# Kernel optimization log

Hardware: AMD Instinct MI355X
Metric: run time of the kernel (lower is better)

## Reference

```python
import jax, jax.numpy as jnp
import numpy as np

B, L, T = 256, 256, 50  # batch, max_len, num_tags


def setup_inputs() -> dict:
    key = jax.random.key(0)
    k1, k2, k3 = jax.random.split(key, 3)
    feats = jax.random.normal(k1, (B, L, T), dtype=jnp.float32)
    trans_m = jax.random.normal(k2, (T, T), dtype=jnp.float32)
    tags = jax.random.randint(k3, (B, L), 0, T)
    mask = jnp.ones((B, L), dtype=jnp.int32)
    return {"feats": feats, "trans_m": trans_m, "tags": tags, "mask": mask}


def _normalizer(logits, trans_m, m):
    # logits: (L, B, T), m: (L, B) float mask
    alpha0 = logits[0]  # (B, T)

    def step(alpha, inp):
        emit, mt = inp  # (B, T), (B,)
        # (B, T_from, T_to) broadcast add, logsumexp over T_from
        tmp = alpha[:, :, None] + trans_m[None, :, :] + emit[:, None, :]
        new = jax.nn.logsumexp(tmp, axis=1)
        alpha = jnp.where(mt[:, None] > 0, new, alpha)
        return alpha, None

    alpha, _ = jax.lax.scan(step, alpha0, (logits[1:], m[1:]))
    return jax.nn.logsumexp(alpha, axis=1)  # (B,)


def _gold_score(logits, trans_m, tags_t, m):
    # logits: (L, B, T); tags_t: (L, B); m: (L, B)
    trans_sc = trans_m[tags_t[:-1], tags_t[1:]] * m[1:]  # (L-1, B)
    emit_sc = jnp.take_along_axis(logits, tags_t[:, :, None], axis=2)[..., 0] * m  # (L, B)
    return jnp.sum(trans_sc + emit_sc[:-1], axis=0) + emit_sc[-1]  # (B,)


def reference(feats, trans_m, tags, mask):
    # feats: (B, L, T) -> (L, B, T); include_start_end_trans=False
    logits = jnp.transpose(feats, (1, 0, 2))
    tags_t = tags.T
    m = mask.T.astype(feats.dtype)
    all_path = _normalizer(logits, trans_m, m)
    gold = _gold_score(logits, trans_m, tags_t, m)
    return all_path - gold  # (B,) loss per example
```

## Files before the change

### kernel.cpp

```cpp
#include <hip/hip_runtime.h>
#include <math.h>


#define TAGS 50
#define LEN 256
#define NB 256
#define TOTF (NB * LEN * TAGS)
#define INV_LN2 1.4426950408889634f
#define LN2 0.6931471805599453f

typedef __attribute__((ext_vector_type(8))) short bf16x8;
typedef __attribute__((ext_vector_type(4))) float f32x4;
typedef __attribute__((ext_vector_type(4), aligned(4))) float f32x4u;

#if __has_builtin(__builtin_amdgcn_exp2f)
#define EXP2F(x) __builtin_amdgcn_exp2f(x)
#else
#define EXP2F(x) exp2f(x)
#endif
#if __has_builtin(__builtin_amdgcn_logf)
#define LOG2F(x) __builtin_amdgcn_logf(x)
#else
#define LOG2F(x) log2f(x)
#endif
#if __has_builtin(__builtin_amdgcn_rcpf)
#define RCPF(x) __builtin_amdgcn_rcpf(x)
#else
#define RCPF(x) (1.0f / (x))
#endif

__device__ __forceinline__ float readlane_f(float v, int srclane) {
  return __builtin_bit_cast(float,
      __builtin_amdgcn_readlane(__builtin_bit_cast(int, v), srclane));
}

__device__ __forceinline__ int bf16pairInit(float lo, float hi) {
  unsigned lb = (__builtin_bit_cast(unsigned, lo) + 0x8000u) >> 16;
  unsigned hb = (__builtin_bit_cast(unsigned, hi) + 0x8000u) & 0xFFFF0000u;
  return (int)(hb | lb);
}

__device__ __forceinline__ float bf16f(unsigned short u) {
  return __builtin_bit_cast(float, ((unsigned)u) << 16);
}

#define PACK2(dst, lo, hi) \
  asm("v_cvt_pk_bf16_f32 %0, %1, %2" : "=v"(dst) : "v"(lo), "v"(hi))

union U8 { int i[4]; bf16x8 v; };

__global__ __launch_bounds__(512, 1) void crf_seg_kernel(
    const float* __restrict__ feats,
    const float* __restrict__ trans,
    const int*   __restrict__ tags,
    const int*   __restrict__ mask,
    float*       __restrict__ out)
{
  const int b    = blockIdx.x;
  const int tid  = threadIdx.x;
  const int w    = tid >> 6;
  const int lane = tid & 63;
  const int q    = lane >> 4;
  const int n    = lane & 15;

  __shared__ __align__(16) unsigned short Plds[6][64][64];
  __shared__ __align__(16) float u_lds[64];
  __shared__ __align__(16) float w_lds[64];
  __shared__ float Sseg[8];
  __shared__ float norm_s, gold_s;

  const int* mbp = mask + b * LEN;
  const unsigned long long mb0 = __ballot(mbp[lane] > 0);
  const unsigned long long mb1 = __ballot(mbp[64 + lane] > 0);
  const unsigned long long mb2 = __ballot(mbp[128 + lane] > 0);
  const unsigned long long mb3 = __ballot(mbp[192 + lane] > 0);
#define MASKBIT(L)                                                          \
  ((int)(((((L) & 128) ? (((L) & 64) ? mb3 : mb2)                           \
                       : (((L) & 64) ? mb1 : mb0)) >> ((L) & 63)) & 1ull))

  U8 Afr[4][2];
#pragma unroll
  for (int t = 0; t < 4; ++t)
#pragma unroll
    for (int c = 0; c < 2; ++c)
#pragma unroll
      for (int r = 0; r < 4; ++r) {
        const int col = 16 * t + n;
        const int tag0 = 16 * c + 4 * q + r;
        const int tag1 = tag0 + 32;
        float e0 = 0.0f, e1 = 0.0f;
        if (col < TAGS) {
          if (tag0 < TAGS) e0 = EXP2F(trans[tag0 * TAGS + col] * INV_LN2);
          if (tag1 < TAGS) e1 = EXP2F(trans[tag1 * TAGS + col] * INV_LN2);
        }
        Afr[t][c].i[r] = bf16pairInit(e0, e1);
      }

  const f32x4 zero4 = {0.0f, 0.0f, 0.0f, 0.0f};

  f32x4 d[4][4];
#pragma unroll
  for (int J = 0; J < 4; ++J)
#pragma unroll
    for (int I = 0; I < 4; ++I)
#pragma unroll
      for (int r = 0; r < 4; ++r)
        d[J][I][r] = (16 * J + n == 16 * I + 4 * q + r) ? 1.0f : 0.0f;

  const int l0 = 32 * w + 1;
  float S = 0.0f;
  f32x4u rA[4], rB[4];

#define LOADG(BK, L) do {                                                   \
    const float* _p = feats + (size_t)b * (LEN * TAGS) + (size_t)(L) * TAGS;\
    BK[0] = *(const f32x4u*)(_p + 4 * q);                                   \
    BK[1] = *(const f32x4u*)(_p + 16 + 4 * q);                              \
    BK[2] = *(const f32x4u*)(_p + 32 + 4 * q);                              \
    const float* _p3 = _p + 46 + 4 * q;                                     \
    const float* _lim = feats + (TOTF - 4);                                 \
    if (_p3 > _lim) _p3 = _lim;                                             \
    BK[3] = *(const f32x4u*)_p3;                                            \
  } while (0)

#define RENORMM() do {                                                      \
    const float _cc = readlane_f(d[0][0][0], 0);                            \
    const float _rr = RCPF(_cc);                                            \
    S += LOG2F(_cc);                                                        \
    _Pragma("unroll") for (int _J = 0; _J < 4; ++_J)                        \
    _Pragma("unroll") for (int _I = 0; _I < 4; ++_I)                        \
    _Pragma("unroll") for (int _r = 0; _r < 4; ++_r)                        \
      d[_J][_I][_r] *= _rr;                                                 \
  } while (0)

#define STEPM(EH, L) do {                                                   \
    if (MASKBIT(L)) {                                                       \
      float ev[4][4];                                                       \
      _Pragma("unroll") for (int _i = 0; _i < 3; ++_i)                      \
      _Pragma("unroll") for (int _r = 0; _r < 4; ++_r)                      \
        ev[_i][_r] = EXP2F(EH[_i][_r] * INV_LN2);                           \
      ev[3][0] = EXP2F(EH[3][2] * INV_LN2);                                 \
      ev[3][1] = EXP2F(EH[3][3] * INV_LN2);                                 \
      ev[3][2] = 0.0f; ev[3][3] = 0.0f;                                     \
      _Pragma("unroll") for (int _J = 0; _J < 4; ++_J) {                    \
        U8 B0, B1;                                                          \
        _Pragma("unroll") for (int _r = 0; _r < 4; ++_r) {                  \
          PACK2(B0.i[_r], d[_J][0][_r], d[_J][2][_r]);                      \
          PACK2(B1.i[_r], d[_J][1][_r], d[_J][3][_r]);                      \
        }                                                                   \
        f32x4 t0 = __builtin_amdgcn_mfma_f32_16x16x32_bf16(Afr[0][1].v, B1.v, zero4, 0, 0, 0); \
        f32x4 t1 = __builtin_amdgcn_mfma_f32_16x16x32_bf16(Afr[1][1].v, B1.v, zero4, 0, 0, 0); \
        f32x4 t2 = __builtin_amdgcn_mfma_f32_16x16x32_bf16(Afr[2][1].v, B1.v, zero4, 0, 0, 0); \
        f32x4 t3 = __builtin_amdgcn_mfma_f32_16x16x32_bf16(Afr[3][1].v, B1.v, zero4, 0, 0, 0); \
        t0 = __builtin_amdgcn_mfma_f32_16x16x32_bf16(Afr[0][0].v, B0.v, t0, 0, 0, 0); \
        t1 = __builtin_amdgcn_mfma_f32_16x16x32_bf16(Afr[1][0].v, B0.v, t1, 0, 0, 0); \
        t2 = __builtin_amdgcn_mfma_f32_16x16x32_bf16(Afr[2][0].v, B0.v, t2, 0, 0, 0); \
        t3 = __builtin_amdgcn_mfma_f32_16x16x32_bf16(Afr[3][0].v, B0.v, t3, 0, 0, 0); \
        _Pragma("unroll") for (int _r = 0; _r < 4; ++_r) {                  \
          d[_J][0][_r] = t0[_r] * ev[0][_r];                                \
          d[_J][1][_r] = t1[_r] * ev[1][_r];                                \
          d[_J][2][_r] = t2[_r] * ev[2][_r];                                \
          d[_J][3][_r] = t3[_r] * ev[3][_r];                                \
        }                                                                   \
      }                                                                     \
    }                                                                       \
  } while (0)

  LOADG(rA, l0);
  LOADG(rB, l0 + 1);

  for (int k = 0; k < 15; ++k) {
    const int l = l0 + 2 * k;
    if ((k & 1) == 0) RENORMM();
    STEPM(rA, l);
    { const int rl = (l + 2 < 255) ? l + 2 : 255; LOADG(rA, rl); }
    STEPM(rB, l + 1);
    { const int rl = (l + 3 < 255) ? l + 3 : 255; LOADG(rB, rl); }
  }
  STEPM(rA, l0 + 30);
  if (w != 7) STEPM(rB, l0 + 31);

  if (lane == 0) Sseg[w] = S;

  if (w == 0) {
    float v0v[4];
#pragma unroll
    for (int J = 0; J < 4; ++J) {
      const int tg = 16 * J + n;
      const float f = feats[(size_t)b * (LEN * TAGS) + tg];
      v0v[J] = (tg < TAGS) ? EXP2F(f * INV_LN2) : 0.0f;
    }
    float pu[4][4];
#pragma unroll
    for (int I = 0; I < 4; ++I)
#pragma unroll
      for (int r = 0; r < 4; ++r)
        pu[I][r] = v0v[0] * d[0][I][r] + v0v[1] * d[1][I][r] +
                   v0v[2] * d[2][I][r] + v0v[3] * d[3][I][r];
#pragma unroll
    for (int off = 1; off <= 8; off <<= 1)
#pragma unroll
      for (int I = 0; I < 4; ++I)
#pragma unroll
        for (int r = 0; r < 4; ++r)
          pu[I][r] += __shfl_xor(pu[I][r], off, 64);
    if (n == 0) {
#pragma unroll
      for (int I = 0; I < 4; ++I)
#pragma unroll
        for (int r = 0; r < 4; ++r)
          u_lds[16 * I + 4 * q + r] = pu[I][r];
    }
  } else if (w == 7) {
    float pw[4];
#pragma unroll
    for (int J = 0; J < 4; ++J) {
      float s = 0.0f;
#pragma unroll
      for (int I = 0; I < 4; ++I)
#pragma unroll
        for (int r = 0; r < 4; ++r)
          s += d[J][I][r];
      pw[J] = s;
    }
#pragma unroll
    for (int J = 0; J < 4; ++J) {
      pw[J] += __shfl_xor(pw[J], 16, 64);
      pw[J] += __shfl_xor(pw[J], 32, 64);
    }
    if (q == 0) {
#pragma unroll
      for (int J = 0; J < 4; ++J) w_lds[16 * J + n] = pw[J];
    }
  } else {
#pragma unroll
    for (int J = 0; J < 4; ++J)
#pragma unroll
      for (int I = 0; I < 4; ++I) {
        int lo, hi;
        PACK2(lo, d[J][I][0], d[J][I][1]);
        PACK2(hi, d[J][I][2], d[J][I][3]);
        unsigned* dst = (unsigned*)&Plds[w - 1][16 * J + n][16 * I + 4 * q];
        dst[0] = (unsigned)lo;
        dst[1] = (unsigned)hi;
      }
  }

  __syncthreads();

  if (w == 0) {
    float x = u_lds[lane];
    float stot = 0.0f;
    for (int j = 0; j < 6; ++j) {
      u_lds[lane] = x;
      asm volatile("s_waitcnt lgkmcnt(0)" ::: "memory");
      float y0 = 0.0f, y1 = 0.0f, y2 = 0.0f, y3 = 0.0f;
#pragma unroll 4
      for (int r = 0; r < 64; r += 4) {
        y0 += u_lds[r]     * bf16f(Plds[j][r][lane]);
        y1 += u_lds[r + 1] * bf16f(Plds[j][r + 1][lane]);
        y2 += u_lds[r + 2] * bf16f(Plds[j][r + 2][lane]);
        y3 += u_lds[r + 3] * bf16f(Plds[j][r + 3][lane]);
      }
      float y = (y0 + y1) + (y2 + y3);
      const float cc = readlane_f(y, 0);
      stot += LOG2F(cc);
      x = y * RCPF(cc);
      asm volatile("s_waitcnt lgkmcnt(0)" ::: "memory");
    }
    float dotv = x * w_lds[lane];
#pragma unroll
    for (int off = 32; off; off >>= 1) dotv += __shfl_xor(dotv, off, 64);
    if (lane == 0) {
      float Ssum = 0.0f;
#pragma unroll
      for (int i = 0; i < 8; ++i) Ssum += Sseg[i];
      norm_s = LN2 * (Ssum + stot + LOG2F(dotv));
    }
  } else if (w == 1) {
    const float* fb = feats + (size_t)b * (LEN * TAGS);
    const int* tb = tags + b * LEN;
    float gp = 0.0f;
#pragma unroll
    for (int k = 0; k < 4; ++k) {
      const int p = lane + 64 * k;
      const int tg = tb[p];
      if (mbp[p] > 0) {
        float vv = fb[p * TAGS + tg];
        if (p >= 1) vv += trans[tb[p - 1] * TAGS + tg];
        gp += vv;
      }
    }
#pragma unroll
    for (int off = 32; off; off >>= 1) gp += __shfl_xor(gp, off, 64);
    if (lane == 0) gold_s = gp;
  }

  __syncthreads();
  if (tid == 0) out[b] = norm_s - gold_s;

#undef MASKBIT
#undef LOADG
#undef RENORMM
#undef STEPM
}

extern "C" void kernel_launch(void* const* d_in, const int* in_sizes, int n_in,
                              void* d_out, int out_size, void* d_ws, size_t ws_size,
                              hipStream_t stream) {
  const float* feats = (const float*)d_in[0];
  const float* trans = (const float*)d_in[1];
  const int*   tags  = (const int*)d_in[2];
  const int*   mask  = (const int*)d_in[3];
  float* out = (float*)d_out;
  (void)d_ws; (void)ws_size;

  crf_seg_kernel<<<NB, 512, 0, stream>>>(feats, trans, tags, mask, out);
}
```

Measured before the change: 106.1 us.

## Split CRF normalizer into forward and backward half-chains with separate combine kernel

```diff
diff --git a/kernel.cpp b/kernel.cpp
--- a/kernel.cpp
+++ b/kernel.cpp
@@ -40,34 +40,33 @@
   return (int)(hb | lb);
 }
 
-__device__ __forceinline__ float bf16f(unsigned short u) {
-  return __builtin_bit_cast(float, ((unsigned)u) << 16);
-}
-
 #define PACK2(dst, lo, hi) \
   asm("v_cvt_pk_bf16_f32 %0, %1, %2" : "=v"(dst) : "v"(lo), "v"(hi))
 
 union U8 { int i[4]; bf16x8 v; };
 
-__global__ __launch_bounds__(512, 1) void crf_seg_kernel(
+#define WS_U(b)  ((b) * 64)
+#define WS_W(b)  ((NB + (b)) * 64)
+#define WS_SF(b) (2 * NB * 64 + (b))
+#define WS_SB(b) (2 * NB * 64 + NB + (b))
+
+__global__ __launch_bounds__(512, 4) void crf_seg_kernel(
     const float* __restrict__ feats,
     const float* __restrict__ trans,
-    const int*   __restrict__ tags,
     const int*   __restrict__ mask,
-    float*       __restrict__ out)
+    float*       __restrict__ ws)
 {
-  const int b    = blockIdx.x;
-  const int tid  = threadIdx.x;
-  const int w    = tid >> 6;
-  const int lane = tid & 63;
-  const int q    = lane >> 4;
-  const int n    = lane & 15;
-
-  __shared__ __align__(16) unsigned short Plds[6][64][64];
-  __shared__ __align__(16) float u_lds[64];
-  __shared__ __align__(16) float w_lds[64];
+  const int bid    = blockIdx.x;
+  const bool is_fwd = bid < NB;
+  const int b      = is_fwd ? bid : bid - NB;
+  const int tid    = threadIdx.x;
+  const int w      = tid >> 6;
+  const int lane   = tid & 63;
+  const int q      = lane >> 4;
+  const int n      = lane & 15;
+
+  __shared__ __align__(16) float x_lds[64];
   __shared__ float Sseg[8];
-  __shared__ float norm_s, gold_s;
 
   const int* mbp = mask + b * LEN;
   const unsigned long long mb0 = __ballot(mbp[lane] > 0);
@@ -90,8 +89,12 @@
         const int tag1 = tag0 + 32;
         float e0 = 0.0f, e1 = 0.0f;
         if (col < TAGS) {
-          if (tag0 < TAGS) e0 = EXP2F(trans[tag0 * TAGS + col] * INV_LN2);
-          if (tag1 < TAGS) e1 = EXP2F(trans[tag1 * TAGS + col] * INV_LN2);
+          if (tag0 < TAGS)
+            e0 = EXP2F((is_fwd ? trans[tag0 * TAGS + col]
+                               : trans[col * TAGS + tag0]) * INV_LN2);
+          if (tag1 < TAGS)
+            e1 = EXP2F((is_fwd ? trans[tag1 * TAGS + col]
+                               : trans[col * TAGS + tag1]) * INV_LN2);
         }
         Afr[t][c].i[r] = bf16pairInit(e0, e1);
       }
@@ -107,7 +110,6 @@
       for (int r = 0; r < 4; ++r)
         d[J][I][r] = (16 * J + n == 16 * I + 4 * q + r) ? 1.0f : 0.0f;
 
-  const int l0 = 32 * w + 1;
   float S = 0.0f;
   f32x4u rA[4], rB[4];
 
@@ -132,29 +134,35 @@
       d[_J][_I][_r] *= _rr;                                                 \
   } while (0)
 
-#define STEPM(EH, L) do {                                                   \
-    if (MASKBIT(L)) {                                                       \
-      float ev[4][4];                                                       \
-      _Pragma("unroll") for (int _i = 0; _i < 3; ++_i)                      \
-      _Pragma("unroll") for (int _r = 0; _r < 4; ++_r)                      \
-        ev[_i][_r] = EXP2F(EH[_i][_r] * INV_LN2);                           \
-      ev[3][0] = EXP2F(EH[3][2] * INV_LN2);                                 \
-      ev[3][1] = EXP2F(EH[3][3] * INV_LN2);                                 \
-      ev[3][2] = 0.0f; ev[3][3] = 0.0f;                                     \
+#define MKEV(EH)                                                            \
+    float ev[4][4];                                                         \
+    _Pragma("unroll") for (int _i = 0; _i < 3; ++_i)                        \
+    _Pragma("unroll") for (int _r = 0; _r < 4; ++_r)                        \
+      ev[_i][_r] = EXP2F(EH[_i][_r] * INV_LN2);                             \
+    ev[3][0] = EXP2F(EH[3][2] * INV_LN2);                                   \
+    ev[3][1] = EXP2F(EH[3][3] * INV_LN2);                                   \
+    ev[3][2] = 0.0f; ev[3][3] = 0.0f
+
+#define MFMA8J(B0_, B1_)                                                    \
+    f32x4 t0 = __builtin_amdgcn_mfma_f32_16x16x32_bf16(Afr[0][1].v, B1_.v, zero4, 0, 0, 0); \
+    f32x4 t1 = __builtin_amdgcn_mfma_f32_16x16x32_bf16(Afr[1][1].v, B1_.v, zero4, 0, 0, 0); \
+    f32x4 t2 = __builtin_amdgcn_mfma_f32_16x16x32_bf16(Afr[2][1].v, B1_.v, zero4, 0, 0, 0); \
+    f32x4 t3 = __builtin_amdgcn_mfma_f32_16x16x32_bf16(Afr[3][1].v, B1_.v, zero4, 0, 0, 0); \
+    t0 = __builtin_amdgcn_mfma_f32_16x16x32_bf16(Afr[0][0].v, B0_.v, t0, 0, 0, 0); \
+    t1 = __builtin_amdgcn_mfma_f32_16x16x32_bf16(Afr[1][0].v, B0_.v, t1, 0, 0, 0); \
+    t2 = __builtin_amdgcn_mfma_f32_16x16x32_bf16(Afr[2][0].v, B0_.v, t2, 0, 0, 0); \
+    t3 = __builtin_amdgcn_mfma_f32_16x16x32_bf16(Afr[3][0].v, B0_.v, t3, 0, 0, 0)
+
+#define STEPF(EH, L) do {                                                   \
+    if ((L) <= 127 && MASKBIT(L)) {                                         \
+      MKEV(EH);                                                             \
       _Pragma("unroll") for (int _J = 0; _J < 4; ++_J) {                    \
         U8 B0, B1;                                                          \
         _Pragma("unroll") for (int _r = 0; _r < 4; ++_r) {                  \
           PACK2(B0.i[_r], d[_J][0][_r], d[_J][2][_r]);                      \
           PACK2(B1.i[_r], d[_J][1][_r], d[_J][3][_r]);                      \
         }                                                                   \
-        f32x4 t0 = __builtin_amdgcn_mfma_f32_16x16x32_bf16(Afr[0][1].v, B1.v, zero4, 0, 0, 0); \
-        f32x4 t1 = __builtin_amdgcn_mfma_f32_16x16x32_bf16(Afr[1][1].v, B1.v, zero4, 0, 0, 0); \
-        f32x4 t2 = __builtin_amdgcn_mfma_f32_16x16x32_bf16(Afr[2][1].v, B1.v, zero4, 0, 0, 0); \
-        f32x4 t3 = __builtin_amdgcn_mfma_f32_16x16x32_bf16(Afr[3][1].v, B1.v, zero4, 0, 0, 0); \
-        t0 = __builtin_amdgcn_mfma_f32_16x16x32_bf16(Afr[0][0].v, B0.v, t0, 0, 0, 0); \
-        t1 = __builtin_amdgcn_mfma_f32_16x16x32_bf16(Afr[1][0].v, B0.v, t1, 0, 0, 0); \
-        t2 = __builtin_amdgcn_mfma_f32_16x16x32_bf16(Afr[2][0].v, B0.v, t2, 0, 0, 0); \
-        t3 = __builtin_amdgcn_mfma_f32_16x16x32_bf16(Afr[3][0].v, B0.v, t3, 0, 0, 0); \
+        MFMA8J(B0, B1);                                                     \
         _Pragma("unroll") for (int _r = 0; _r < 4; ++_r) {                  \
           d[_J][0][_r] = t0[_r] * ev[0][_r];                                \
           d[_J][1][_r] = t1[_r] * ev[1][_r];                                \
@@ -165,143 +173,196 @@
     }                                                                       \
   } while (0)
 
-  LOADG(rA, l0);
-  LOADG(rB, l0 + 1);
-
-  for (int k = 0; k < 15; ++k) {
-    const int l = l0 + 2 * k;
-    if ((k & 1) == 0) RENORMM();
-    STEPM(rA, l);
-    { const int rl = (l + 2 < 255) ? l + 2 : 255; LOADG(rA, rl); }
-    STEPM(rB, l + 1);
-    { const int rl = (l + 3 < 255) ? l + 3 : 255; LOADG(rB, rl); }
+#define STEPB(EH, L) do {                                                   \
+    if (MASKBIT(L)) {                                                       \
+      MKEV(EH);                                                             \
+      _Pragma("unroll") for (int _J = 0; _J < 4; ++_J) {                    \
+        U8 B0, B1;                                                          \
+        _Pragma("unroll") for (int _r = 0; _r < 4; ++_r) {                  \
+          PACK2(B0.i[_r], ev[0][_r] * d[_J][0][_r], ev[2][_r] * d[_J][2][_r]); \
+          PACK2(B1.i[_r], ev[1][_r] * d[_J][1][_r], ev[3][_r] * d[_J][3][_r]); \
+        }                                                                   \
+        MFMA8J(B0, B1);                                                     \
+        _Pragma("unroll") for (int _r = 0; _r < 4; ++_r) {                  \
+          d[_J][0][_r] = t0[_r];                                            \
+          d[_J][1][_r] = t1[_r];                                            \
+          d[_J][2][_r] = t2[_r];                                            \
+          d[_J][3][_r] = t3[_r];                                            \
+        }                                                                   \
+      }                                                                     \
+    }                                                                       \
+  } while (0)
+
+  if (is_fwd) {
+    int l = 1 + 16 * w;
+    LOADG(rA, l);
+    LOADG(rB, l + 1);
+    for (int kk = 0; kk < 8; ++kk) {
+      if ((kk & 1) == 0) RENORMM();
+      STEPF(rA, l); LOADG(rA, l + 2);
+      ++l;
+      STEPF(rB, l); LOADG(rB, l + 2);
+      ++l;
+    }
+  } else {
+    int l = 143 + 16 * w;
+    LOADG(rA, l);
+    LOADG(rB, l - 1);
+    for (int kk = 0; kk < 8; ++kk) {
+      if ((kk & 1) == 0) RENORMM();
+      STEPB(rA, l); LOADG(rA, l - 2);
+      --l;
+      STEPB(rB, l); LOADG(rB, l - 2);
+      --l;
+    }
   }
-  STEPM(rA, l0 + 30);
-  if (w != 7) STEPM(rB, l0 + 31);
-
-  if (lane == 0) Sseg[w] = S;
-
-  if (w == 0) {
-    float v0v[4];
-#pragma unroll
-    for (int J = 0; J < 4; ++J) {
-      const int tg = 16 * J + n;
-      const float f = feats[(size_t)b * (LEN * TAGS) + tg];
-      v0v[J] = (tg < TAGS) ? EXP2F(f * INV_LN2) : 0.0f;
-    }
-    float pu[4][4];
-#pragma unroll
-    for (int I = 0; I < 4; ++I)
-#pragma unroll
-      for (int r = 0; r < 4; ++r)
-        pu[I][r] = v0v[0] * d[0][I][r] + v0v[1] * d[1][I][r] +
-                   v0v[2] * d[2][I][r] + v0v[3] * d[3][I][r];
-#pragma unroll
-    for (int off = 1; off <= 8; off <<= 1)
-#pragma unroll
-      for (int I = 0; I < 4; ++I)
-#pragma unroll
-        for (int r = 0; r < 4; ++r)
-          pu[I][r] += __shfl_xor(pu[I][r], off, 64);
-    if (n == 0) {
-#pragma unroll
-      for (int I = 0; I < 4; ++I)
-#pragma unroll
-        for (int r = 0; r < 4; ++r)
-          u_lds[16 * I + 4 * q + r] = pu[I][r];
-    }
-  } else if (w == 7) {
-    float pw[4];
-#pragma unroll
-    for (int J = 0; J < 4; ++J) {
+
+  __syncthreads();
+
+  if (is_fwd) {
+    for (int f = 0; f < 8; ++f) {
+      if (w == f) {
+        float xv[4];
+        if (f == 0) {
+#pragma unroll
+          for (int J = 0; J < 4; ++J) {
+            const int tg = 16 * J + n;
+            xv[J] = (tg < TAGS)
+                        ? EXP2F(feats[(size_t)b * (LEN * TAGS) + tg] * INV_LN2)
+                        : 0.0f;
+          }
+        } else {
+#pragma unroll
+          for (int J = 0; J < 4; ++J) xv[J] = x_lds[16 * J + n];
+        }
+        float p[4][4];
+#pragma unroll
+        for (int I = 0; I < 4; ++I)
+#pragma unroll
+          for (int r = 0; r < 4; ++r)
+            p[I][r] = xv[0] * d[0][I][r] + xv[1] * d[1][I][r] +
+                      xv[2] * d[2][I][r] + xv[3] * d[3][I][r];
+#pragma unroll
+        for (int off = 1; off <= 8; off <<= 1)
+#pragma unroll
+          for (int I = 0; I < 4; ++I)
+#pragma unroll
+            for (int r = 0; r < 4; ++r)
+              p[I][r] += __shfl_xor(p[I][r], off, 64);
+        const float cc = readlane_f(p[0][0], 0);
+        const float rr = RCPF(cc);
+        S += LOG2F(cc);
+        if (n == 0) {
+#pragma unroll
+          for (int I = 0; I < 4; ++I)
+#pragma unroll
+            for (int r = 0; r < 4; ++r)
+              x_lds[16 * I + 4 * q + r] = p[I][r] * rr;
+        }
+        if (lane == 0) Sseg[w] = S;
+      }
+      __syncthreads();
+    }
+    if (tid < 64) ws[WS_U(b) + tid] = x_lds[tid];
+    if (tid == 0) {
       float s = 0.0f;
 #pragma unroll
-      for (int I = 0; I < 4; ++I)
-#pragma unroll
-        for (int r = 0; r < 4; ++r)
-          s += d[J][I][r];
-      pw[J] = s;
-    }
-#pragma unroll
-    for (int J = 0; J < 4; ++J) {
-      pw[J] += __shfl_xor(pw[J], 16, 64);
-      pw[J] += __shfl_xor(pw[J], 32, 64);
-    }
-    if (q == 0) {
-#pragma unroll
-      for (int J = 0; J < 4; ++J) w_lds[16 * J + n] = pw[J];
+      for (int i = 0; i < 8; ++i) s += Sseg[i];
+      ws[WS_SF(b)] = s;
     }
   } else {
-#pragma unroll
-    for (int J = 0; J < 4; ++J)
-#pragma unroll
-      for (int I = 0; I < 4; ++I) {
-        int lo, hi;
-        PACK2(lo, d[J][I][0], d[J][I][1]);
-        PACK2(hi, d[J][I][2], d[J][I][3]);
-        unsigned* dst = (unsigned*)&Plds[w - 1][16 * J + n][16 * I + 4 * q];
-        dst[0] = (unsigned)lo;
-        dst[1] = (unsigned)hi;
+    for (int f2 = 0; f2 < 8; ++f2) {
+      if (w == 7 - f2) {
+        float xv[4];
+        if (w == 7) {
+#pragma unroll
+          for (int J = 0; J < 4; ++J) xv[J] = (16 * J + n < TAGS) ? 1.0f : 0.0f;
+        } else {
+#pragma unroll
+          for (int J = 0; J < 4; ++J) xv[J] = x_lds[16 * J + n];
+        }
+        float t[4][4];
+#pragma unroll
+        for (int I = 0; I < 4; ++I)
+#pragma unroll
+          for (int r = 0; r < 4; ++r)
+            t[I][r] = xv[0] * d[0][I][r] + xv[1] * d[1][I][r] +
+                      xv[2] * d[2][I][r] + xv[3] * d[3][I][r];
+#pragma unroll
+        for (int off = 1; off <= 8; off <<= 1)
+#pragma unroll
+          for (int I = 0; I < 4; ++I)
+#pragma unroll
+            for (int r = 0; r < 4; ++r)
+              t[I][r] += __shfl_xor(t[I][r], off, 64);
+        const float cc = readlane_f(t[0][0], 0);
+        const float rr = RCPF(cc);
+        S += LOG2F(cc);
+        if (n == 0) {
+#pragma unroll
+          for (int I = 0; I < 4; ++I)
+#pragma unroll
+            for (int r = 0; r < 4; ++r)
+              x_lds[16 * I + 4 * q + r] = t[I][r] * rr;
+        }
+        if (lane == 0) Sseg[w] = S;
       }
+      __syncthreads();
+    }
+    if (tid < 64) ws[WS_W(b) + tid] = x_lds[tid];
+    if (tid == 0) {
+      float s = 0.0f;
+#pragma unroll
+      for (int i = 0; i < 8; ++i) s += Sseg[i];
+      ws[WS_SB(b)] = s;
+    }
   }
-
-  __syncthreads();
-
-  if (w == 0) {
-    float x = u_lds[lane];
-    float stot = 0.0f;
-    for (int j = 0; j < 6; ++j) {
-      u_lds[lane] = x;
-      asm volatile("s_waitcnt lgkmcnt(0)" ::: "memory");
-      float y0 = 0.0f, y1 = 0.0f, y2 = 0.0f, y3 = 0.0f;
-#pragma unroll 4
-      for (int r = 0; r < 64; r += 4) {
-        y0 += u_lds[r]     * bf16f(Plds[j][r][lane]);
-        y1 += u_lds[r + 1] * bf16f(Plds[j][r + 1][lane]);
-        y2 += u_lds[r + 2] * bf16f(Plds[j][r + 2][lane]);
-        y3 += u_lds[r + 3] * bf16f(Plds[j][r + 3][lane]);
-      }
-      float y = (y0 + y1) + (y2 + y3);
-      const float cc = readlane_f(y, 0);
-      stot += LOG2F(cc);
-      x = y * RCPF(cc);
-      asm volatile("s_waitcnt lgkmcnt(0)" ::: "memory");
-    }
-    float dotv = x * w_lds[lane];
-#pragma unroll
-    for (int off = 32; off; off >>= 1) dotv += __shfl_xor(dotv, off, 64);
-    if (lane == 0) {
-      float Ssum = 0.0f;
-#pragma unroll
-      for (int i = 0; i < 8; ++i) Ssum += Sseg[i];
-      norm_s = LN2 * (Ssum + stot + LOG2F(dotv));
-    }
-  } else if (w == 1) {
-    const float* fb = feats + (size_t)b * (LEN * TAGS);
-    const int* tb = tags + b * LEN;
-    float gp = 0.0f;
-#pragma unroll
-    for (int k = 0; k < 4; ++k) {
-      const int p = lane + 64 * k;
-      const int tg = tb[p];
-      if (mbp[p] > 0) {
-        float vv = fb[p * TAGS + tg];
-        if (p >= 1) vv += trans[tb[p - 1] * TAGS + tg];
-        gp += vv;
-      }
-    }
-#pragma unroll
-    for (int off = 32; off; off >>= 1) gp += __shfl_xor(gp, off, 64);
-    if (lane == 0) gold_s = gp;
-  }
-
-  __syncthreads();
-  if (tid == 0) out[b] = norm_s - gold_s;
-
 #undef MASKBIT
 #undef LOADG
 #undef RENORMM
-#undef STEPM
+#undef MKEV
+#undef MFMA8J
+#undef STEPF
+#undef STEPB
+}
+
+__global__ __launch_bounds__(64) void crf_combine_kernel(
+    const float* __restrict__ feats,
+    const float* __restrict__ trans,
+    const int*   __restrict__ tags,
+    const int*   __restrict__ mask,
+    const float* __restrict__ ws,
+    float*       __restrict__ out)
+{
+  const int b = blockIdx.x;
+  const int lane = threadIdx.x;
+
+  float s = ws[WS_U(b) + lane] * ws[WS_W(b) + lane];
+#pragma unroll
+  for (int off = 32; off; off >>= 1) s += __shfl_xor(s, off, 64);
+
+  const float* fb = feats + (size_t)b * (LEN * TAGS);
+  const int*   tb = tags + b * LEN;
+  const int*   mb = mask + b * LEN;
+  float gp = 0.0f;
+#pragma unroll
+  for (int k = 0; k < 4; ++k) {
+    const int p = lane + 64 * k;
+    const int tg = tb[p];
+    if (mb[p] > 0) {
+      float vv = fb[p * TAGS + tg];
+      if (p >= 1) vv += trans[tb[p - 1] * TAGS + tg];
+      gp += vv;
+    }
+  }
+#pragma unroll
+  for (int off = 32; off; off >>= 1) gp += __shfl_xor(gp, off, 64);
+
+  if (lane == 0) {
+    const float Sf = ws[WS_SF(b)];
+    const float Sb = ws[WS_SB(b)];
+    out[b] = LN2 * (Sf + Sb + LOG2F(s)) - gp;
+  }
 }
 
 extern "C" void kernel_launch(void* const* d_in, const int* in_sizes, int n_in,
@@ -312,7 +373,8 @@
   const int*   tags  = (const int*)d_in[2];
   const int*   mask  = (const int*)d_in[3];
   float* out = (float*)d_out;
-  (void)d_ws; (void)ws_size;
-
-  crf_seg_kernel<<<NB, 512, 0, stream>>>(feats, trans, tags, mask, out);
-}
+  float* ws  = (float*)d_ws;
+
+  crf_seg_kernel<<<2 * NB, 512, 0, stream>>>(feats, trans, mask, ws);
+  crf_combine_kernel<<<NB, 64, 0, stream>>>(feats, trans, tags, mask, ws, out);
+}
```

After: 304.9 us. +187.3%, slower.
